# Kernel tuning notes

Measured on AMD Instinct MI355X. Metric: run time of the kernel, lower is better.

The kernel has to match this reference:

```python
import jax, jax.numpy as jnp
import numpy as np

B, S, D, E, K = 4, 2048, 1024, 8, 2
H = 4 * D  # SwiGLU hidden size


def setup_inputs() -> dict:
    key = jax.random.key(0)
    ks = jax.random.split(key, 6)
    s = 0.02
    return {
        "x": jax.random.normal(ks[0], (B, S, D), dtype=jnp.float32),
        "Wr": jax.random.normal(ks[1], (D, E), dtype=jnp.float32) * s,
        "br": jnp.zeros((E,), jnp.float32),
        "Wg": jax.random.normal(ks[2], (E, D, H), dtype=jnp.float32) * s,
        "bg": jnp.zeros((E, H), jnp.float32),
        "Wu": jax.random.normal(ks[3], (E, D, H), dtype=jnp.float32) * s,
        "bu": jnp.zeros((E, H), jnp.float32),
        "Wd": jax.random.normal(ks[4], (E, H, D), dtype=jnp.float32) * s,
        "bd": jnp.zeros((E, D), jnp.float32),
        "top_k": K,
    }


def reference(x, Wr, br, Wg, bg, Wu, bu, Wd, bd, top_k):
    # Router: top-k over expert logits, softmax over the selected k values.
    Bx, Sx, Dx = x.shape
    Ex = Wr.shape[-1]
    logits = x @ Wr + br                              # [B,S,E]
    vals, idx = jax.lax.top_k(logits, top_k)          # [B,S,K]
    probs = jax.nn.softmax(vals, axis=-1)             # [B,S,K]
    # Dense per-token expert weight; 0 for experts the token is not routed to.
    gate_w = jnp.sum(jax.nn.one_hot(idx, Ex, dtype=x.dtype) * probs[..., None], axis=-2)  # [B,S,E]

    xt = x.reshape(-1, Dx)          # [T,D]
    gw = gate_w.reshape(-1, Ex).T   # [E,T]

    def body(acc, p):
        wg, bgi, wu, bui, wd, bdi, ge = p
        h = jax.nn.silu(xt @ wg + bgi) * (xt @ wu + bui)   # [T,4D]
        y = (h @ wd + bdi) * ge[:, None]                   # zero where ge==0 (not routed)
        return acc + y, None

    out, _ = jax.lax.scan(body, jnp.zeros_like(xt), (Wg, bg, Wu, bu, Wd, bd, gw))
    return out.reshape(Bx, Sx, Dx)
```

## Files before the change

kernel.cpp:

```cpp
#include <hip/hip_runtime.h>
#include <hip/hip_fp16.h>


#define T_TOK 8192
#define D_IN  1024
#define E_EXP 8
#define H_HID 4096
#define NSLOT (T_TOK * 2)
#define NSLOT_PAD (NSLOT + 128)

typedef _Float16 f16;
typedef __attribute__((ext_vector_type(8))) _Float16 f16x8;
typedef __attribute__((ext_vector_type(4))) _Float16 f16x4;
typedef __attribute__((ext_vector_type(4))) float f32x4;

__device__ __forceinline__ void gload_lds16(const void* g, void* l) {
  __builtin_amdgcn_global_load_lds(
      (const __attribute__((address_space(1))) unsigned int*)g,
      (__attribute__((address_space(3))) unsigned int*)l, 16, 0, 0);
}


__global__ __launch_bounds__(256) void convert_x_kernel(
    const float* __restrict__ x, f16* __restrict__ xb, int n4) {
  int i = blockIdx.x * 256 + threadIdx.x;
  if (i >= n4) return;
  float4 v = ((const float4*)x)[i];
  f16x4 o = {(f16)v.x, (f16)v.y, (f16)v.z, (f16)v.w};
  *(f16x4*)(xb + (size_t)i * 4) = o;
}

__global__ __launch_bounds__(256) void transpose_cvt_kernel(
    const float* __restrict__ src, f16* __restrict__ dst, int R, int C) {
  __shared__ float tile[32][33];
  int b = blockIdx.z;
  const float* s = src + (size_t)b * R * C;
  f16* d = dst + (size_t)b * R * C;
  int c0 = blockIdx.x * 32, r0 = blockIdx.y * 32;
  int tr = threadIdx.x >> 3;
  int tc4 = (threadIdx.x & 7) * 4;
  float4 v = *(const float4*)(s + (size_t)(r0 + tr) * C + c0 + tc4);
  tile[tr][tc4 + 0] = v.x;
  tile[tr][tc4 + 1] = v.y;
  tile[tr][tc4 + 2] = v.z;
  tile[tr][tc4 + 3] = v.w;
  __syncthreads();
  f16x4 o = {(f16)tile[tc4 + 0][tr], (f16)tile[tc4 + 1][tr],
             (f16)tile[tc4 + 2][tr], (f16)tile[tc4 + 3][tr]};
  *(f16x4*)(d + (size_t)(c0 + tr) * R + r0 + tc4) = o;
}


__global__ __launch_bounds__(256) void router_kernel(
    const float* __restrict__ x, const float* __restrict__ Wr,
    const float* __restrict__ br, int* __restrict__ eidx,
    float2* __restrict__ pval, int* __restrict__ counts) {
  int lane = threadIdx.x & 63, wid = threadIdx.x >> 6;
  int t = blockIdx.x * 4 + wid;
  const float* xr = x + (size_t)t * D_IN;
  float s[8] = {0.f, 0.f, 0.f, 0.f, 0.f, 0.f, 0.f, 0.f};
  int dbase = lane * 16;
#pragma unroll
  for (int i = 0; i < 4; ++i) {
    float4 xv = *(const float4*)(xr + dbase + i * 4);
    const float xs[4] = {xv.x, xv.y, xv.z, xv.w};
#pragma unroll
    for (int j = 0; j < 4; ++j) {
      const float* wr = Wr + (size_t)(dbase + i * 4 + j) * E_EXP;
      float4 w0 = *(const float4*)wr;
      float4 w1 = *(const float4*)(wr + 4);
      float xvj = xs[j];
      s[0] += xvj * w0.x; s[1] += xvj * w0.y; s[2] += xvj * w0.z; s[3] += xvj * w0.w;
      s[4] += xvj * w1.x; s[5] += xvj * w1.y; s[6] += xvj * w1.z; s[7] += xvj * w1.w;
    }
  }
#pragma unroll
  for (int off = 32; off; off >>= 1)
#pragma unroll
    for (int e = 0; e < 8; ++e) s[e] += __shfl_xor(s[e], off);
  if (lane == 0) {
    float v[8];
#pragma unroll
    for (int e = 0; e < 8; ++e) v[e] = s[e] + br[e];
    int i0 = 0; float v0 = v[0];
#pragma unroll
    for (int e = 1; e < 8; ++e) if (v[e] > v0) { v0 = v[e]; i0 = e; }
    int i1 = -1; float v1 = -1e30f;
#pragma unroll
    for (int e = 0; e < 8; ++e)
      if (e != i0 && v[e] > v1) { v1 = v[e]; i1 = e; }
    float ed = __expf(v1 - v0);
    float inv = 1.f / (1.f + ed);
    eidx[t] = i0 | (i1 << 8);
    pval[t] = make_float2(inv, ed * inv);
    atomicAdd(&counts[i0], 1);
    atomicAdd(&counts[i1], 1);
  }
}

__global__ void scan_kernel(const int* __restrict__ counts, int* __restrict__ offsets) {
  if (threadIdx.x == 0) {
    int acc = 0;
#pragma unroll
    for (int e = 0; e < E_EXP; ++e) { offsets[e] = acc; acc += counts[e]; }
    offsets[E_EXP] = acc;
  }
}

__global__ __launch_bounds__(256) void scatter_kernel(
    const int* __restrict__ eidx, const float2* __restrict__ pval,
    const int* __restrict__ offsets, int* __restrict__ cursors,
    int* __restrict__ perm, float* __restrict__ gatew, int2* __restrict__ slotAB) {
  int t = blockIdx.x * 256 + threadIdx.x;
  if (t >= T_TOK) return;
  int ei = eidx[t];
  float2 p = pval[t];
  int e0 = ei & 0xff, e1 = (ei >> 8) & 0xff;
  int s0 = offsets[e0] + atomicAdd(&cursors[e0], 1);
  perm[s0] = t; gatew[s0] = p.x;
  int s1 = offsets[e1] + atomicAdd(&cursors[e1], 1);
  perm[s1] = t; gatew[s1] = p.y;
  slotAB[t] = make_int2(s0, s1);
}

__global__ __launch_bounds__(256, 2) void ffn1_kernel(
    const f16* __restrict__ xb, const f16* __restrict__ wgt,
    const f16* __restrict__ wut, const float* __restrict__ bg,
    const float* __restrict__ bu, const int* __restrict__ offsets,
    const int* __restrict__ perm, f16* __restrict__ hbuf) {
  __shared__ f16 aT[128 * 64];
  __shared__ f16 bgT[128 * 64];
  __shared__ f16 buT[128 * 64];
  int e = blockIdx.z;
  int off = offsets[e];
  int cnt = offsets[e + 1] - off;
  int mt = blockIdx.y;
  if (mt * 128 >= cnt) return;
  int n0 = blockIdx.x * 128;
  int tid = threadIdx.x, lane = tid & 63, wid = tid >> 6;
  int wr = wid >> 1, wc = wid & 1;
  int l15 = lane & 15, lc0 = lane >> 4;

  const f16 *gA[4], *gG[4], *gU[4];
#pragma unroll
  for (int i = 0; i < 4; ++i) {
    int linear = i * 256 + tid;
    int row = linear >> 3, p = linear & 7;
    int lc = p ^ (row & 7);
    int srow = min(off + mt * 128 + row, off + cnt - 1);
    gA[i] = xb + (size_t)perm[srow] * D_IN + lc * 8;
    gG[i] = wgt + (size_t)e * H_HID * D_IN + (size_t)(n0 + row) * D_IN + lc * 8;
    gU[i] = wut + (size_t)e * H_HID * D_IN + (size_t)(n0 + row) * D_IN + lc * 8;
  }

  f32x4 accg[4][4] = {};
  f32x4 accu[4][4] = {};

  for (int kt = 0; kt < D_IN / 64; ++kt) {
    __syncthreads();
#pragma unroll
    for (int i = 0; i < 4; ++i) {
      gload_lds16(gA[i] + kt * 64, &aT[(i * 256 + wid * 64) * 8]);
      gload_lds16(gG[i] + kt * 64, &bgT[(i * 256 + wid * 64) * 8]);
      gload_lds16(gU[i] + kt * 64, &buT[(i * 256 + wid * 64) * 8]);
    }
    __syncthreads();
#pragma unroll
    for (int kk = 0; kk < 2; ++kk) {
      int c = kk * 4 + lc0;
      f16x8 af[4];
#pragma unroll
      for (int m = 0; m < 4; ++m) {
        int r = wr * 64 + m * 16 + l15;
        af[m] = *(const f16x8*)&aT[r * 64 + (c ^ (r & 7)) * 8];
      }
#pragma unroll
      for (int n = 0; n < 4; ++n) {
        int r = wc * 64 + n * 16 + l15;
        int o8 = r * 64 + (c ^ (r & 7)) * 8;
        f16x8 bgf = *(const f16x8*)&bgT[o8];
#pragma unroll
        for (int m = 0; m < 4; ++m)
          accg[m][n] = __builtin_amdgcn_mfma_f32_16x16x32_f16(af[m], bgf, accg[m][n], 0, 0, 0);
        f16x8 buf_ = *(const f16x8*)&buT[o8];
#pragma unroll
        for (int m = 0; m < 4; ++m)
          accu[m][n] = __builtin_amdgcn_mfma_f32_16x16x32_f16(af[m], buf_, accu[m][n], 0, 0, 0);
      }
    }
  }

#pragma unroll
  for (int n = 0; n < 4; ++n) {
    int h = n0 + wc * 64 + n * 16 + l15;
    float bgv = bg[e * H_HID + h];
    float buv = bu[e * H_HID + h];
#pragma unroll
    for (int m = 0; m < 4; ++m) {
#pragma unroll
      for (int r = 0; r < 4; ++r) {
        int local = mt * 128 + wr * 64 + m * 16 + lc0 * 4 + r;
        if (local < cnt) {
          float g = accg[m][n][r] + bgv;
          float u = accu[m][n][r] + buv;
          hbuf[(size_t)(off + local) * H_HID + h] = (f16)((g / (1.f + __expf(-g))) * u);
        }
      }
    }
  }
}

__global__ __launch_bounds__(256, 2) void ffn2_kernel(
    const f16* __restrict__ hbuf, const f16* __restrict__ wdt,
    const float* __restrict__ bd, const int* __restrict__ offsets,
    const float* __restrict__ gatew, f16* __restrict__ ybuf) {
  __shared__ f16 aT[128 * 64];
  __shared__ f16 bT[128 * 64];
  int e = blockIdx.z;
  int off = offsets[e];
  int cnt = offsets[e + 1] - off;
  int mt = blockIdx.y;
  if (mt * 128 >= cnt) return;
  int n0 = blockIdx.x * 128;
  int tid = threadIdx.x, lane = tid & 63, wid = tid >> 6;
  int wr = wid >> 1, wc = wid & 1;
  int l15 = lane & 15, lc0 = lane >> 4;
  const f16* gaBase = hbuf + (size_t)(off + mt * 128) * H_HID;
  const f16* gbBase = wdt + (size_t)e * D_IN * H_HID;

  const f16 *gA[4], *gB[4];
#pragma unroll
  for (int i = 0; i < 4; ++i) {
    int linear = i * 256 + tid;
    int row = linear >> 3, p = linear & 7;
    int lc = p ^ (row & 7);
    gA[i] = gaBase + (size_t)row * H_HID + lc * 8;
    gB[i] = gbBase + (size_t)(n0 + row) * H_HID + lc * 8;
  }

  f32x4 acc[4][4] = {};

  for (int kt = 0; kt < H_HID / 64; ++kt) {
    __syncthreads();
#pragma unroll
    for (int i = 0; i < 4; ++i) {
      gload_lds16(gA[i] + kt * 64, &aT[(i * 256 + wid * 64) * 8]);
      gload_lds16(gB[i] + kt * 64, &bT[(i * 256 + wid * 64) * 8]);
    }
    __syncthreads();
#pragma unroll
    for (int kk = 0; kk < 2; ++kk) {
      int c = kk * 4 + lc0;
      f16x8 af[4];
#pragma unroll
      for (int m = 0; m < 4; ++m) {
        int r = wr * 64 + m * 16 + l15;
        af[m] = *(const f16x8*)&aT[r * 64 + (c ^ (r & 7)) * 8];
      }
#pragma unroll
      for (int n = 0; n < 4; ++n) {
        int r = wc * 64 + n * 16 + l15;
        f16x8 bf = *(const f16x8*)&bT[r * 64 + (c ^ (r & 7)) * 8];
#pragma unroll
        for (int m = 0; m < 4; ++m)
          acc[m][n] = __builtin_amdgcn_mfma_f32_16x16x32_f16(af[m], bf, acc[m][n], 0, 0, 0);
      }
    }
  }

#pragma unroll
  for (int n = 0; n < 4; ++n) {
    int col = n0 + wc * 64 + n * 16 + l15;
    float bdv = bd[e * D_IN + col];
#pragma unroll
    for (int m = 0; m < 4; ++m) {
#pragma unroll
      for (int r = 0; r < 4; ++r) {
        int local = mt * 128 + wr * 64 + m * 16 + lc0 * 4 + r;
        if (local < cnt) {
          int slot = off + local;
          ybuf[(size_t)slot * D_IN + col] = (f16)(gatew[slot] * (acc[m][n][r] + bdv));
        }
      }
    }
  }
}

__global__ __launch_bounds__(256) void combine_kernel(
    const f16* __restrict__ ybuf, const int2* __restrict__ slotAB,
    float* __restrict__ out) {
  int i = blockIdx.x * 256 + threadIdx.x;
  int t = i >> 7;
  int c8 = i & 127;
  int2 s = slotAB[t];
  f16x8 y0 = *(const f16x8*)(ybuf + (size_t)s.x * D_IN + c8 * 8);
  f16x8 y1 = *(const f16x8*)(ybuf + (size_t)s.y * D_IN + c8 * 8);
  float* o = out + (size_t)t * D_IN + c8 * 8;
  float4 o0 = make_float4((float)y0[0] + (float)y1[0], (float)y0[1] + (float)y1[1],
                          (float)y0[2] + (float)y1[2], (float)y0[3] + (float)y1[3]);
  float4 o1 = make_float4((float)y0[4] + (float)y1[4], (float)y0[5] + (float)y1[5],
                          (float)y0[6] + (float)y1[6], (float)y0[7] + (float)y1[7]);
  ((float4*)o)[0] = o0;
  ((float4*)o)[1] = o1;
}


extern "C" void kernel_launch(void* const* d_in, const int* in_sizes, int n_in,
                              void* d_out, int out_size, void* d_ws, size_t ws_size,
                              hipStream_t stream) {
  const float* x  = (const float*)d_in[0];
  const float* Wr = (const float*)d_in[1];
  const float* br = (const float*)d_in[2];
  const float* Wg = (const float*)d_in[3];
  const float* bg = (const float*)d_in[4];
  const float* Wu = (const float*)d_in[5];
  const float* bu = (const float*)d_in[6];
  const float* Wd = (const float*)d_in[7];
  const float* bd = (const float*)d_in[8];
  float* out = (float*)d_out;

  char* ws = (char*)d_ws;
  size_t o = 0;
  auto alloc = [&](size_t bytes) {
    size_t r = o;
    o += (bytes + 255) & ~(size_t)255;
    return r;
  };
  f16* xb     = (f16*)(ws + alloc((size_t)T_TOK * D_IN * 2));
  f16* wgt    = (f16*)(ws + alloc((size_t)E_EXP * H_HID * D_IN * 2));
  f16* wut    = (f16*)(ws + alloc((size_t)E_EXP * H_HID * D_IN * 2));
  f16* wdt    = (f16*)(ws + alloc((size_t)E_EXP * D_IN * H_HID * 2));
  f16* hbuf   = (f16*)(ws + alloc((size_t)NSLOT_PAD * H_HID * 2));
  int* eidx   = (int*)(ws + alloc((size_t)T_TOK * 4));
  float2* pval= (float2*)(ws + alloc((size_t)T_TOK * 8));
  int* counts = (int*)(ws + alloc(64 * 4));
  int* cursors = counts + 8;
  int* offsets = counts + 16;
  int* perm   = (int*)(ws + alloc((size_t)NSLOT_PAD * 4));
  float* gatew= (float*)(ws + alloc((size_t)NSLOT_PAD * 4));
  int2* slotAB= (int2*)(ws + alloc((size_t)T_TOK * 8));
  f16* ybuf   = wgt;

  hipMemsetAsync(counts, 0, 64 * 4, stream);

  convert_x_kernel<<<(T_TOK * D_IN / 4 + 255) / 256, 256, 0, stream>>>(
      x, xb, T_TOK * D_IN / 4);
  transpose_cvt_kernel<<<dim3(H_HID / 32, D_IN / 32, E_EXP), 256, 0, stream>>>(
      Wg, wgt, D_IN, H_HID);
  transpose_cvt_kernel<<<dim3(H_HID / 32, D_IN / 32, E_EXP), 256, 0, stream>>>(
      Wu, wut, D_IN, H_HID);
  transpose_cvt_kernel<<<dim3(D_IN / 32, H_HID / 32, E_EXP), 256, 0, stream>>>(
      Wd, wdt, H_HID, D_IN);
  router_kernel<<<T_TOK / 4, 256, 0, stream>>>(x, Wr, br, eidx, pval, counts);
  scan_kernel<<<1, 64, 0, stream>>>(counts, offsets);
  scatter_kernel<<<T_TOK / 256, 256, 0, stream>>>(eidx, pval, offsets, cursors,
                                                  perm, gatew, slotAB);
  ffn1_kernel<<<dim3(H_HID / 128, 128, E_EXP), 256, 0, stream>>>(
      xb, wgt, wut, bg, bu, offsets, perm, hbuf);
  ffn2_kernel<<<dim3(D_IN / 128, 128, E_EXP), 256, 0, stream>>>(
      hbuf, wdt, bd, offsets, gatew, ybuf);
  combine_kernel<<<T_TOK * D_IN / 8 / 256, 256, 0, stream>>>(ybuf, slotAB, out);
}
```

Baseline: 1.075 ms.

## Replace FFN GEMMs with 256x256-tile 8-phase pipelined kernel and interleaved gate/up weights

Both expert GEMMs now use a single templated kernel with 512 threads, 256x256 output tiles, double-buffered 128KB LDS, and an eight-phase schedule. That schedule interleaves async global-to-LDS loads with MFMA quadrants, separated by explicit barriers and setprio. Gate and up weights are transposed into one buffer, interleaved in 16-row groups, so a single B tile yields matched gate/up columns for the SwiGLU epilogue. The aim is better MFMA utilisation and more operand reuse by hiding load latency and enlarging tiles. The cost is much higher LDS and register pressure, and more wasted work on partially filled 256-row tiles at expert boundaries.

Result: no change. 1.054 ms (-1.9%).

```diff
diff --git a/kernel.cpp b/kernel.cpp
--- a/kernel.cpp
+++ b/kernel.cpp
@@ -7,7 +7,7 @@
 #define E_EXP 8
 #define H_HID 4096
 #define NSLOT (T_TOK * 2)
-#define NSLOT_PAD (NSLOT + 128)
+#define NSLOT_PAD (NSLOT + 256)
 
 typedef _Float16 f16;
 typedef __attribute__((ext_vector_type(8))) _Float16 f16x8;
@@ -30,12 +30,14 @@
   *(f16x4*)(xb + (size_t)i * 4) = o;
 }
 
+template<int MAP>
 __global__ __launch_bounds__(256) void transpose_cvt_kernel(
-    const float* __restrict__ src, f16* __restrict__ dst, int R, int C) {
+    const float* __restrict__ src, f16* __restrict__ dst, int R, int C,
+    size_t dstride) {
   __shared__ float tile[32][33];
   int b = blockIdx.z;
   const float* s = src + (size_t)b * R * C;
-  f16* d = dst + (size_t)b * R * C;
+  f16* d = dst + (size_t)b * dstride;
   int c0 = blockIdx.x * 32, r0 = blockIdx.y * 32;
   int tr = threadIdx.x >> 3;
   int tc4 = (threadIdx.x & 7) * 4;
@@ -45,9 +47,11 @@
   tile[tr][tc4 + 2] = v.z;
   tile[tr][tc4 + 3] = v.w;
   __syncthreads();
+  int c = c0 + tr;
+  int ro = (MAP == 0) ? c : (((c >> 4) << 5) + ((MAP == 2) ? 16 : 0) + (c & 15));
   f16x4 o = {(f16)tile[tc4 + 0][tr], (f16)tile[tc4 + 1][tr],
              (f16)tile[tc4 + 2][tr], (f16)tile[tc4 + 3][tr]};
-  *(f16x4*)(d + (size_t)(c0 + tr) * R + r0 + tc4) = o;
+  *(f16x4*)(d + (size_t)ro * R + r0 + tc4) = o;
 }
 
 
@@ -123,163 +127,157 @@
   slotAB[t] = make_int2(s0, s1);
 }
 
-__global__ __launch_bounds__(256, 2) void ffn1_kernel(
-    const f16* __restrict__ xb, const f16* __restrict__ wgt,
-    const f16* __restrict__ wut, const float* __restrict__ bg,
-    const float* __restrict__ bu, const int* __restrict__ offsets,
-    const int* __restrict__ perm, f16* __restrict__ hbuf) {
-  __shared__ f16 aT[128 * 64];
-  __shared__ f16 bgT[128 * 64];
-  __shared__ f16 buT[128 * 64];
-  int e = blockIdx.z;
+
+#define SB0 __builtin_amdgcn_sched_barrier(0)
+#define BAR do { SB0; __builtin_amdgcn_s_barrier(); SB0; } while (0)
+
+#define STAGE_(B, ISB, H, KT, BASE) do {                                   \
+  char* d_ = smem + (B)*65536 + (ISB)*32768 + (H)*16384 + wid*1024;        \
+  gload_lds16(BASE[(H)*2+0] + (size_t)(KT)*64, d_);                        \
+  gload_lds16(BASE[(H)*2+1] + (size_t)(KT)*64, d_ + 8192);                 \
+} while (0)
+
+#define LDA_(B, Q)                                                          \
+  _Pragma("unroll")                                                         \
+  for (int m_ = 0; m_ < 4; ++m_) {                                          \
+    fa[m_][0] = *(const f16x8*)(smem + (B)*65536 + aoff + ((Q)*4+m_)*2048 + offk0); \
+    fa[m_][1] = *(const f16x8*)(smem + (B)*65536 + aoff + ((Q)*4+m_)*2048 + offk1); \
+  }
+
+#define LDB_(FB, B, RH)                                                     \
+  _Pragma("unroll")                                                         \
+  for (int n_ = 0; n_ < 2; ++n_) {                                          \
+    FB[n_][0] = *(const f16x8*)(smem + (B)*65536 + 32768 + boff + ((RH)*2+n_)*2048 + offk0); \
+    FB[n_][1] = *(const f16x8*)(smem + (B)*65536 + 32768 + boff + ((RH)*2+n_)*2048 + offk1); \
+  }
+
+#define QUAD_(Q, RH, FB)                                                    \
+  __builtin_amdgcn_s_setprio(1);                                            \
+  _Pragma("unroll")                                                         \
+  for (int m_ = 0; m_ < 4; ++m_)                                            \
+    _Pragma("unroll")                                                       \
+    for (int n_ = 0; n_ < 2; ++n_) {                                        \
+      acc[(Q)*4+m_][(RH)*2+n_] = __builtin_amdgcn_mfma_f32_16x16x32_f16(    \
+          fa[m_][0], FB[n_][0], acc[(Q)*4+m_][(RH)*2+n_], 0, 0, 0);         \
+      acc[(Q)*4+m_][(RH)*2+n_] = __builtin_amdgcn_mfma_f32_16x16x32_f16(    \
+          fa[m_][1], FB[n_][1], acc[(Q)*4+m_][(RH)*2+n_], 0, 0, 0);         \
+    }                                                                       \
+  __builtin_amdgcn_s_setprio(0);
+
+template<int MODE>
+__global__ __launch_bounds__(512, 2) void ffn_8ph_kernel(
+    const f16* __restrict__ Asrc, const f16* __restrict__ Bsrc,
+    const float* __restrict__ bias0, const float* __restrict__ bias1,
+    const int* __restrict__ offsets, const int* __restrict__ perm,
+    const float* __restrict__ gatew, f16* __restrict__ dst) {
+  constexpr int KD = MODE ? H_HID : D_IN;
+  constexpr int BROWS = MODE ? D_IN : 2 * H_HID;
+  constexpr int NT = KD / 64;
+  static_assert(NT % 2 == 0, "NT even");
+
+  __shared__ __align__(16) char smem[131072];
+
+  int nt = blockIdx.x, e = blockIdx.y, mt = blockIdx.z;
   int off = offsets[e];
   int cnt = offsets[e + 1] - off;
-  int mt = blockIdx.y;
-  if (mt * 128 >= cnt) return;
-  int n0 = blockIdx.x * 128;
+  if (mt * 256 >= cnt) return;
+
   int tid = threadIdx.x, lane = tid & 63, wid = tid >> 6;
-  int wr = wid >> 1, wc = wid & 1;
-  int l15 = lane & 15, lc0 = lane >> 4;
-
-  const f16 *gA[4], *gG[4], *gU[4];
-#pragma unroll
-  for (int i = 0; i < 4; ++i) {
-    int linear = i * 256 + tid;
-    int row = linear >> 3, p = linear & 7;
-    int lc = p ^ (row & 7);
-    int srow = min(off + mt * 128 + row, off + cnt - 1);
-    gA[i] = xb + (size_t)perm[srow] * D_IN + lc * 8;
-    gG[i] = wgt + (size_t)e * H_HID * D_IN + (size_t)(n0 + row) * D_IN + lc * 8;
-    gU[i] = wut + (size_t)e * H_HID * D_IN + (size_t)(n0 + row) * D_IN + lc * 8;
-  }
-
-  f32x4 accg[4][4] = {};
-  f32x4 accu[4][4] = {};
-
-  for (int kt = 0; kt < D_IN / 64; ++kt) {
-    __syncthreads();
-#pragma unroll
-    for (int i = 0; i < 4; ++i) {
-      gload_lds16(gA[i] + kt * 64, &aT[(i * 256 + wid * 64) * 8]);
-      gload_lds16(gG[i] + kt * 64, &bgT[(i * 256 + wid * 64) * 8]);
-      gload_lds16(gU[i] + kt * 64, &buT[(i * 256 + wid * 64) * 8]);
+  int wm = wid >> 2, wn = wid & 3;
+  int l15 = lane & 15, lc0 = lane >> 4, s7 = l15 & 7;
+  int aoff = (wm * 128 + l15) * 128;
+  int boff = (wn * 64 + l15) * 128;
+  int offk0 = ((lc0) ^ s7) * 16;
+  int offk1 = ((lc0 + 4) ^ s7) * 16;
+
+  const f16 *aB[4], *bB[4];
+#pragma unroll
+  for (int h = 0; h < 2; ++h)
+#pragma unroll
+    for (int i = 0; i < 2; ++i) {
+      int chunk = (i * 8 + wid) * 64 + lane;
+      int rowh = chunk >> 3;
+      int lc = (chunk & 7) ^ (rowh & 7);
+      int absrow = h * 128 + rowh;
+      int slot = off + min(mt * 256 + absrow, cnt - 1);
+      if constexpr (MODE == 0)
+        aB[h * 2 + i] = Asrc + (size_t)perm[slot] * KD + lc * 8;
+      else
+        aB[h * 2 + i] = Asrc + (size_t)slot * KD + lc * 8;
+      bB[h * 2 + i] = Bsrc + ((size_t)e * BROWS + nt * 256 + absrow) * KD + lc * 8;
     }
-    __syncthreads();
-#pragma unroll
-    for (int kk = 0; kk < 2; ++kk) {
-      int c = kk * 4 + lc0;
-      f16x8 af[4];
-#pragma unroll
-      for (int m = 0; m < 4; ++m) {
-        int r = wr * 64 + m * 16 + l15;
-        af[m] = *(const f16x8*)&aT[r * 64 + (c ^ (r & 7)) * 8];
-      }
-#pragma unroll
-      for (int n = 0; n < 4; ++n) {
-        int r = wc * 64 + n * 16 + l15;
-        int o8 = r * 64 + (c ^ (r & 7)) * 8;
-        f16x8 bgf = *(const f16x8*)&bgT[o8];
-#pragma unroll
-        for (int m = 0; m < 4; ++m)
-          accg[m][n] = __builtin_amdgcn_mfma_f32_16x16x32_f16(af[m], bgf, accg[m][n], 0, 0, 0);
-        f16x8 buf_ = *(const f16x8*)&buT[o8];
-#pragma unroll
-        for (int m = 0; m < 4; ++m)
-          accu[m][n] = __builtin_amdgcn_mfma_f32_16x16x32_f16(af[m], buf_, accu[m][n], 0, 0, 0);
-      }
-    }
-  }
-
-#pragma unroll
-  for (int n = 0; n < 4; ++n) {
-    int h = n0 + wc * 64 + n * 16 + l15;
-    float bgv = bg[e * H_HID + h];
-    float buv = bu[e * H_HID + h];
-#pragma unroll
-    for (int m = 0; m < 4; ++m) {
-#pragma unroll
-      for (int r = 0; r < 4; ++r) {
-        int local = mt * 128 + wr * 64 + m * 16 + lc0 * 4 + r;
-        if (local < cnt) {
-          float g = accg[m][n][r] + bgv;
-          float u = accu[m][n][r] + buv;
-          hbuf[(size_t)(off + local) * H_HID + h] = (f16)((g / (1.f + __expf(-g))) * u);
+
+  f32x4 acc[8][4] = {};
+  f16x8 fa[4][2], fb01[2][2], fb23[2][2];
+
+  STAGE_(0, 1, 0, 0, bB); STAGE_(0, 1, 1, 0, bB);
+  STAGE_(0, 0, 0, 0, aB); STAGE_(0, 0, 1, 0, aB);
+  STAGE_(1, 1, 0, 1, bB); STAGE_(1, 1, 1, 1, bB);
+  asm volatile("s_waitcnt vmcnt(4)" ::: "memory");
+  BAR;
+
+  for (int it = 0; it < NT / 2; ++it) {
+    int t1 = 2 * it + 1;
+    int t2 = min(2 * it + 2, NT - 1);
+    int t3 = min(2 * it + 3, NT - 1);
+    LDA_(0, 0); LDB_(fb01, 0, 0); STAGE_(1, 0, 0, t1, aB);
+    BAR; QUAD_(0, 0, fb01); BAR;
+    LDB_(fb23, 0, 1); STAGE_(1, 0, 1, t1, aB);
+    BAR; QUAD_(0, 1, fb23); BAR;
+    LDA_(0, 1); STAGE_(0, 1, 0, t2, bB);
+    BAR; QUAD_(1, 0, fb01); BAR;
+    STAGE_(0, 1, 1, t2, bB);
+    asm volatile("s_waitcnt vmcnt(4)" ::: "memory");
+    BAR; QUAD_(1, 1, fb23); BAR;
+    LDA_(1, 0); LDB_(fb01, 1, 0); STAGE_(0, 0, 0, t2, aB);
+    BAR; QUAD_(0, 0, fb01); BAR;
+    LDB_(fb23, 1, 1); STAGE_(0, 0, 1, t2, aB);
+    BAR; QUAD_(0, 1, fb23); BAR;
+    LDA_(1, 1); STAGE_(1, 1, 0, t3, bB);
+    BAR; QUAD_(1, 0, fb01); BAR;
+    STAGE_(1, 1, 1, t3, bB);
+    asm volatile("s_waitcnt vmcnt(4)" ::: "memory");
+    BAR; QUAD_(1, 1, fb23); BAR;
+  }
+
+  asm volatile("s_waitcnt vmcnt(0)" ::: "memory");
+  BAR;
+
+  int c0_ = lc0 * 4;
+  if constexpr (MODE == 0) {
+#pragma unroll
+    for (int p = 0; p < 2; ++p) {
+      int h = nt * 128 + wn * 32 + p * 16 + l15;
+      float bgv = bias0[e * H_HID + h];
+      float buv = bias1[e * H_HID + h];
+#pragma unroll
+      for (int m = 0; m < 8; ++m) {
+        int lbase = mt * 256 + wm * 128 + m * 16 + c0_;
+#pragma unroll
+        for (int r = 0; r < 4; ++r) {
+          if (lbase + r < cnt) {
+            float g = acc[m][2 * p][r] + bgv;
+            float u = acc[m][2 * p + 1][r] + buv;
+            dst[(size_t)(off + lbase + r) * H_HID + h] =
+                (f16)((g / (1.f + __expf(-g))) * u);
+          }
         }
       }
     }
-  }
-}
-
-__global__ __launch_bounds__(256, 2) void ffn2_kernel(
-    const f16* __restrict__ hbuf, const f16* __restrict__ wdt,
-    const float* __restrict__ bd, const int* __restrict__ offsets,
-    const float* __restrict__ gatew, f16* __restrict__ ybuf) {
-  __shared__ f16 aT[128 * 64];
-  __shared__ f16 bT[128 * 64];
-  int e = blockIdx.z;
-  int off = offsets[e];
-  int cnt = offsets[e + 1] - off;
-  int mt = blockIdx.y;
-  if (mt * 128 >= cnt) return;
-  int n0 = blockIdx.x * 128;
-  int tid = threadIdx.x, lane = tid & 63, wid = tid >> 6;
-  int wr = wid >> 1, wc = wid & 1;
-  int l15 = lane & 15, lc0 = lane >> 4;
-  const f16* gaBase = hbuf + (size_t)(off + mt * 128) * H_HID;
-  const f16* gbBase = wdt + (size_t)e * D_IN * H_HID;
-
-  const f16 *gA[4], *gB[4];
-#pragma unroll
-  for (int i = 0; i < 4; ++i) {
-    int linear = i * 256 + tid;
-    int row = linear >> 3, p = linear & 7;
-    int lc = p ^ (row & 7);
-    gA[i] = gaBase + (size_t)row * H_HID + lc * 8;
-    gB[i] = gbBase + (size_t)(n0 + row) * H_HID + lc * 8;
-  }
-
-  f32x4 acc[4][4] = {};
-
-  for (int kt = 0; kt < H_HID / 64; ++kt) {
-    __syncthreads();
-#pragma unroll
-    for (int i = 0; i < 4; ++i) {
-      gload_lds16(gA[i] + kt * 64, &aT[(i * 256 + wid * 64) * 8]);
-      gload_lds16(gB[i] + kt * 64, &bT[(i * 256 + wid * 64) * 8]);
-    }
-    __syncthreads();
-#pragma unroll
-    for (int kk = 0; kk < 2; ++kk) {
-      int c = kk * 4 + lc0;
-      f16x8 af[4];
-#pragma unroll
-      for (int m = 0; m < 4; ++m) {
-        int r = wr * 64 + m * 16 + l15;
-        af[m] = *(const f16x8*)&aT[r * 64 + (c ^ (r & 7)) * 8];
-      }
-#pragma unroll
-      for (int n = 0; n < 4; ++n) {
-        int r = wc * 64 + n * 16 + l15;
-        f16x8 bf = *(const f16x8*)&bT[r * 64 + (c ^ (r & 7)) * 8];
-#pragma unroll
-        for (int m = 0; m < 4; ++m)
-          acc[m][n] = __builtin_amdgcn_mfma_f32_16x16x32_f16(af[m], bf, acc[m][n], 0, 0, 0);
-      }
-    }
-  }
-
-#pragma unroll
-  for (int n = 0; n < 4; ++n) {
-    int col = n0 + wc * 64 + n * 16 + l15;
-    float bdv = bd[e * D_IN + col];
-#pragma unroll
-    for (int m = 0; m < 4; ++m) {
-#pragma unroll
-      for (int r = 0; r < 4; ++r) {
-        int local = mt * 128 + wr * 64 + m * 16 + lc0 * 4 + r;
-        if (local < cnt) {
-          int slot = off + local;
-          ybuf[(size_t)slot * D_IN + col] = (f16)(gatew[slot] * (acc[m][n][r] + bdv));
+  } else {
+#pragma unroll
+    for (int n = 0; n < 4; ++n) {
+      int col = nt * 256 + wn * 64 + n * 16 + l15;
+      float bdv = bias0[e * D_IN + col];
+#pragma unroll
+      for (int m = 0; m < 8; ++m) {
+        int lbase = mt * 256 + wm * 128 + m * 16 + c0_;
+#pragma unroll
+        for (int r = 0; r < 4; ++r) {
+          if (lbase + r < cnt) {
+            int slot = off + lbase + r;
+            dst[(size_t)slot * D_IN + col] = (f16)(gatew[slot] * (acc[m][n][r] + bdv));
+          }
         }
       }
     }
@@ -327,8 +325,7 @@
     return r;
   };
   f16* xb     = (f16*)(ws + alloc((size_t)T_TOK * D_IN * 2));
-  f16* wgt    = (f16*)(ws + alloc((size_t)E_EXP * H_HID * D_IN * 2));
-  f16* wut    = (f16*)(ws + alloc((size_t)E_EXP * H_HID * D_IN * 2));
+  f16* wgut   = (f16*)(ws + alloc((size_t)E_EXP * 2 * H_HID * D_IN * 2));
   f16* wdt    = (f16*)(ws + alloc((size_t)E_EXP * D_IN * H_HID * 2));
   f16* hbuf   = (f16*)(ws + alloc((size_t)NSLOT_PAD * H_HID * 2));
   int* eidx   = (int*)(ws + alloc((size_t)T_TOK * 4));
@@ -339,25 +336,25 @@
   int* perm   = (int*)(ws + alloc((size_t)NSLOT_PAD * 4));
   float* gatew= (float*)(ws + alloc((size_t)NSLOT_PAD * 4));
   int2* slotAB= (int2*)(ws + alloc((size_t)T_TOK * 8));
-  f16* ybuf   = wgt;
+  f16* ybuf   = wgut;
 
   hipMemsetAsync(counts, 0, 64 * 4, stream);
 
   convert_x_kernel<<<(T_TOK * D_IN / 4 + 255) / 256, 256, 0, stream>>>(
       x, xb, T_TOK * D_IN / 4);
-  transpose_cvt_kernel<<<dim3(H_HID / 32, D_IN / 32, E_EXP), 256, 0, stream>>>(
-      Wg, wgt, D_IN, H_HID);
-  transpose_cvt_kernel<<<dim3(H_HID / 32, D_IN / 32, E_EXP), 256, 0, stream>>>(
-      Wu, wut, D_IN, H_HID);
-  transpose_cvt_kernel<<<dim3(D_IN / 32, H_HID / 32, E_EXP), 256, 0, stream>>>(
-      Wd, wdt, H_HID, D_IN);
+  transpose_cvt_kernel<1><<<dim3(H_HID / 32, D_IN / 32, E_EXP), 256, 0, stream>>>(
+      Wg, wgut, D_IN, H_HID, (size_t)2 * H_HID * D_IN);
+  transpose_cvt_kernel<2><<<dim3(H_HID / 32, D_IN / 32, E_EXP), 256, 0, stream>>>(
+      Wu, wgut, D_IN, H_HID, (size_t)2 * H_HID * D_IN);
+  transpose_cvt_kernel<0><<<dim3(D_IN / 32, H_HID / 32, E_EXP), 256, 0, stream>>>(
+      Wd, wdt, H_HID, D_IN, (size_t)D_IN * H_HID);
   router_kernel<<<T_TOK / 4, 256, 0, stream>>>(x, Wr, br, eidx, pval, counts);
   scan_kernel<<<1, 64, 0, stream>>>(counts, offsets);
   scatter_kernel<<<T_TOK / 256, 256, 0, stream>>>(eidx, pval, offsets, cursors,
                                                   perm, gatew, slotAB);
-  ffn1_kernel<<<dim3(H_HID / 128, 128, E_EXP), 256, 0, stream>>>(
-      xb, wgt, wut, bg, bu, offsets, perm, hbuf);
-  ffn2_kernel<<<dim3(D_IN / 128, 128, E_EXP), 256, 0, stream>>>(
-      hbuf, wdt, bd, offsets, gatew, ybuf);
+  ffn_8ph_kernel<0><<<dim3(2 * H_HID / 256, E_EXP, 32), 512, 0, stream>>>(
+      xb, wgut, bg, bu, offsets, perm, nullptr, hbuf);
+  ffn_8ph_kernel<1><<<dim3(D_IN / 256, E_EXP, 32), 512, 0, stream>>>(
+      hbuf, wdt, bd, nullptr, offsets, nullptr, gatew, ybuf);
   combine_kernel<<<T_TOK * D_IN / 8 / 256, 256, 0, stream>>>(ybuf, slotAB, out);
 }
```
